# Performance work log

Measured on AMD Instinct MI355X. Metric: run time of the kernel, lower is better.

The kernel has to match this reference:

```python
import jax, jax.numpy as jnp
import numpy as np

N, E, F_IN, HID, K, CLS = 50000, 800000, 512, 128, 4, 40
EPS = 0.3


def setup_inputs() -> dict:
    key = jax.random.key(0)
    ks = jax.random.split(key, 6)
    x = jax.random.normal(ks[0], (N, F_IN), dtype=jnp.float32)
    edge_index = jax.random.randint(ks[1], (2, E), 0, N, dtype=jnp.int32)
    # xavier_normal with gain=1.414 ~ gain*sqrt(2/(fan_in+fan_out))
    t1_w = jax.random.normal(ks[2], (HID, F_IN), jnp.float32) * (1.414 * np.sqrt(2.0 / (F_IN + HID)))
    t1_b = jnp.zeros((HID,), jnp.float32)
    gate_w = jax.random.normal(ks[3], (K, 2 * HID), jnp.float32) * (1.414 * np.sqrt(2.0 / (2 * HID + 1)))
    gate_b = jnp.zeros((K,), jnp.float32)
    t2_w = jax.random.normal(ks[4], (CLS, HID), jnp.float32) * (1.414 * np.sqrt(2.0 / (HID + CLS)))
    t2_b = jnp.zeros((CLS,), jnp.float32)
    return dict(x=x, edge_index=edge_index, t1_w=t1_w, t1_b=t1_b,
                gate_w=gate_w, gate_b=gate_b, t2_w=t2_w, t2_b=t2_b)


def _fa_layer(h, row, col, nd, gw, gb):
    # gate(cat[h_row, h_col]) as two matvecs (equivalent to concat + Linear)
    d = h.shape[1]
    g = jnp.tanh(h[row] @ gw[:d] + h[col] @ gw[d:] + gb)   # [E]
    norm = g * nd[row] * nd[col]                           # [E]
    msg = norm[:, None] * h[row]                           # x_j = h[source], [E, HID]
    # aggregate (add) into target nodes
    return jax.ops.segment_sum(msg, col, num_segments=h.shape[0])


def reference(x, edge_index, t1_w, t1_b, gate_w, gate_b, t2_w, t2_b):
    row, col = edge_index[0], edge_index[1]
    deg = jax.ops.segment_sum(jnp.ones((E,), x.dtype), row, num_segments=N)
    nd = jnp.clip(deg, 1.0, None) ** -0.5                  # degree^{-1/2}, clamped at 1
    h = jax.nn.relu(x @ t1_w.T + t1_b)                     # [N, HID]
    raw = h
    for k in range(K):
        h = EPS * raw + _fa_layer(h, row, col, nd, gate_w[k], gate_b[k])
    return jax.nn.log_softmax(h @ t2_w.T + t2_b, axis=1)   # [N, CLS]
```

## Files before the change

kernel.cpp:

```cpp
#include <hip/hip_runtime.h>
#include <math.h>

#define N_NODES 50000
#define N_EDGES 800000
#define F_IN    512
#define HID     128
#define K_LAYERS 4
#define N_CLS   40
#define EPS_C   0.3f
#define CAP     64

#define GB_BLOCKS 391
#define PB_BLOCKS 3125

typedef __bf16 bf16x8 __attribute__((ext_vector_type(8)));
typedef float  f32x4  __attribute__((ext_vector_type(4)));
typedef float  f32x2  __attribute__((ext_vector_type(2)));

__device__ inline unsigned short bfb(float f) {
    __bf16 b = (__bf16)f;
    return __builtin_bit_cast(unsigned short, b);
}
__device__ inline unsigned pack2(float a, float b) {
    return (unsigned)bfb(a) | ((unsigned)bfb(b) << 16);
}
__device__ inline float lo2(unsigned v) { return __builtin_bit_cast(float, v << 16); }
__device__ inline float hi2(unsigned v) { return __builtin_bit_cast(float, v & 0xffff0000u); }
__device__ inline bf16x8 ld_frag(const unsigned short* p) {
    uint4 q = *(const uint4*)p;
    return __builtin_bit_cast(bf16x8, q);
}
__device__ inline void acc_fp8(float g, uint2 v, float* acc) {
    f32x2 p0 = __builtin_amdgcn_cvt_pk_f32_fp8((int)v.x, false);
    f32x2 p1 = __builtin_amdgcn_cvt_pk_f32_fp8((int)v.x, true);
    f32x2 p2 = __builtin_amdgcn_cvt_pk_f32_fp8((int)v.y, false);
    f32x2 p3 = __builtin_amdgcn_cvt_pk_f32_fp8((int)v.y, true);
    acc[0] = fmaf(g, p0[0], acc[0]); acc[1] = fmaf(g, p0[1], acc[1]);
    acc[2] = fmaf(g, p1[0], acc[2]); acc[3] = fmaf(g, p1[1], acc[3]);
    acc[4] = fmaf(g, p2[0], acc[4]); acc[5] = fmaf(g, p2[1], acc[5]);
    acc[6] = fmaf(g, p3[0], acc[6]); acc[7] = fmaf(g, p3[1], acc[7]);
}

#define GS 72
__global__ __launch_bounds__(256) void k_gemm_prep(const float* __restrict__ x,
                                                   const float* __restrict__ w,
                                                   const float* __restrict__ bias,
                                                   unsigned* __restrict__ h0b,
                                                   unsigned short* __restrict__ h08,
                                                   const int* __restrict__ row,
                                                   const int* __restrict__ col,
                                                   int* __restrict__ deg,
                                                   int* __restrict__ cur,
                                                   int* __restrict__ bucket) {
    if (blockIdx.x >= GB_BLOCKS) {
        int e = (blockIdx.x - GB_BLOCKS) * 256 + threadIdx.x;
        if (e < N_EDGES) {
            int r = row[e], c = col[e];
            atomicAdd(&deg[r], 1);
            int p = atomicAdd(&cur[c], 1);
            if (p < CAP) bucket[((size_t)c << 6) + p] = r;
        }
        return;
    }

    __shared__ __attribute__((aligned(16))) unsigned short As[128 * GS];
    __shared__ __attribute__((aligned(16))) unsigned short Bs[128 * GS];
    const int t    = threadIdx.x;
    const int lane = t & 63;
    const int wv   = t >> 6;
    const int wrow = wv >> 1;
    const int wcol = wv & 1;
    const int nb0  = blockIdx.x * 128;
    const int m16  = lane & 15;
    const int quad = lane >> 4;

    f32x4 acc[4][4];
#pragma unroll
    for (int mi = 0; mi < 4; mi++)
#pragma unroll
        for (int ni = 0; ni < 4; ni++) acc[mi][ni] = (f32x4){0.f, 0.f, 0.f, 0.f};

    for (int k0 = 0; k0 < F_IN; k0 += 64) {
        __syncthreads();
        {
            int r  = t & 127;
            int kh = (t >> 7) * 32;
            int n  = nb0 + r;
            unsigned short* pl = &As[r * GS + kh];
            if (n < N_NODES) {
                const float* px = &x[(size_t)n * F_IN + k0 + kh];
#pragma unroll
                for (int q = 0; q < 4; q++) {
                    float4 f0 = *(const float4*)(px + q * 8);
                    float4 f1 = *(const float4*)(px + q * 8 + 4);
                    *(ushort4*)(pl + q * 8)     = make_ushort4(bfb(f0.x), bfb(f0.y), bfb(f0.z), bfb(f0.w));
                    *(ushort4*)(pl + q * 8 + 4) = make_ushort4(bfb(f1.x), bfb(f1.y), bfb(f1.z), bfb(f1.w));
                }
            } else {
#pragma unroll
                for (int q = 0; q < 8; q++) *(ushort4*)(pl + q * 4) = make_ushort4(0, 0, 0, 0);
            }
        }
        {
            int j  = t & 127;
            int kh = (t >> 7) * 32;
            const float* pw = &w[(size_t)j * F_IN + k0 + kh];
            unsigned short* pl = &Bs[j * GS + kh];
#pragma unroll
            for (int q = 0; q < 4; q++) {
                float4 f0 = *(const float4*)(pw + q * 8);
                float4 f1 = *(const float4*)(pw + q * 8 + 4);
                *(ushort4*)(pl + q * 8)     = make_ushort4(bfb(f0.x), bfb(f0.y), bfb(f0.z), bfb(f0.w));
                *(ushort4*)(pl + q * 8 + 4) = make_ushort4(bfb(f1.x), bfb(f1.y), bfb(f1.z), bfb(f1.w));
            }
        }
        __syncthreads();
#pragma unroll
        for (int kk = 0; kk < 64; kk += 32) {
            bf16x8 af[4], bfr[4];
#pragma unroll
            for (int mi = 0; mi < 4; mi++)
                af[mi] = ld_frag(&As[(wrow * 64 + mi * 16 + m16) * GS + kk + quad * 8]);
#pragma unroll
            for (int ni = 0; ni < 4; ni++)
                bfr[ni] = ld_frag(&Bs[(wcol * 64 + ni * 16 + m16) * GS + kk + quad * 8]);
#pragma unroll
            for (int mi = 0; mi < 4; mi++)
#pragma unroll
                for (int ni = 0; ni < 4; ni++)
                    acc[mi][ni] = __builtin_amdgcn_mfma_f32_16x16x32_bf16(af[mi], bfr[ni], acc[mi][ni], 0, 0, 0);
        }
    }
    float bj[4];
#pragma unroll
    for (int ni = 0; ni < 4; ni++) bj[ni] = bias[wcol * 64 + ni * 16 + m16];
    unsigned short* h0u = (unsigned short*)h0b;
    unsigned char*  h8u = (unsigned char*)h08;
#pragma unroll
    for (int mi = 0; mi < 4; mi++)
#pragma unroll
        for (int reg = 0; reg < 4; reg++) {
            int n = nb0 + wrow * 64 + mi * 16 + quad * 4 + reg;
            if (n < N_NODES) {
#pragma unroll
                for (int ni = 0; ni < 4; ni++) {
                    float v = fmaxf(acc[mi][ni][reg] + bj[ni], 0.f);
                    int f = wcol * 64 + ni * 16 + m16;
                    h0u[(size_t)n * HID + f] = bfb(v);
                    int pk = __builtin_amdgcn_cvt_pk_fp8_f32(v, v, 0, false);
                    h8u[(size_t)n * HID + f] = (unsigned char)(pk & 0xff);
                }
            }
        }
}

__global__ __launch_bounds__(256) void k_gate0(const unsigned* __restrict__ h0b,
                                               const int* __restrict__ deg,
                                               const float* __restrict__ gw,
                                               float2* __restrict__ pn0,
                                               float* __restrict__ bn0) {
    const int node = blockIdx.x * 4 + (threadIdx.x >> 6);
    const int lane = threadIdx.x & 63;
    if (node >= N_NODES) return;
    unsigned v = h0b[((size_t)node << 6) + lane];
    float hx = lo2(v), hy = hi2(v);
    float pa = hx * gw[2 * lane]       + hy * gw[2 * lane + 1];
    float pb = hx * gw[128 + 2 * lane] + hy * gw[129 + 2 * lane];
#pragma unroll
    for (int d = 32; d > 0; d >>= 1) {
        pa += __shfl_xor(pa, d);
        pb += __shfl_xor(pb, d);
    }
    if (lane == 0) {
        float dv = fmaxf((float)deg[node], 1.0f);
        pn0[node] = make_float2(pa, 1.0f / sqrtf(dv));
        bn0[node] = pb;
    }
}

#define ISSUE_GRP(BASE, A, B, C, D)                                  \
    {                                                                \
        int ea = __shfl(idx, (BASE) + esub);                         \
        int eb = __shfl(idx, (BASE) + esub + 4);                     \
        int ec = __shfl(idx, (BASE) + esub + 8);                     \
        int ed = __shfl(idx, (BASE) + esub + 12);                    \
        A = h8v[(size_t)ea * 16 + fg];                               \
        B = h8v[(size_t)eb * 16 + fg];                               \
        C = h8v[(size_t)ec * 16 + fg];                               \
        D = h8v[(size_t)ed * 16 + fg];                               \
    }

__global__ __launch_bounds__(256) void k_agg7(const unsigned short* __restrict__ h8,
                                              const unsigned* __restrict__ h0b,
                                              const float2* __restrict__ pn,
                                              const float* __restrict__ bn,
                                              const int* __restrict__ bucket,
                                              const int* __restrict__ cur,
                                              const float* __restrict__ gb_all, int k,
                                              unsigned short* __restrict__ out8,
                                              unsigned* __restrict__ out16,
                                              const float* __restrict__ gwn,
                                              float2* __restrict__ pnn,
                                              float* __restrict__ bnn) {
    const int node = blockIdx.x * 4 + (threadIdx.x >> 6);
    const int lane = threadIdx.x & 63;
    if (node >= N_NODES) return;
    const int esub = lane >> 4;
    const int fg   = lane & 15;

    const int    cntr = cur[node];
    int          idx  = bucket[((size_t)node << 6) + lane];
    const float2 pno  = pn[node];
    const float  bwr  = bn[node];
    uint4 h0v = ((const uint4*)h0b)[(size_t)node * 16 + fg];

    const int   cnt = min(cntr, CAP);
    if (lane >= cnt) idx = 0;
    const float ndc = pno.y;
    const float bw  = bwr + gb_all[k];

    const uint2* h8v = (const uint2*)h8;
    uint2 v0 = make_uint2(0, 0), v1 = v0, v2 = v0, v3 = v0;
    uint2 w0 = v0, w1 = v0, w2 = v0, w3 = v0;
    if (cnt > 0)  ISSUE_GRP(0,  v0, v1, v2, v3);
    if (cnt > 16) ISSUE_GRP(16, w0, w1, w2, w3);

    float g = 0.f;
    if (lane < cnt) {
        float2 pr = pn[idx];
        float tt = pr.x + bw;
        float ex = __expf(tt + tt);
        g = (1.f - 2.f / (ex + 1.f)) * pr.y * ndc;
    }

    float acc[8];
#pragma unroll
    for (int j = 0; j < 8; j++) acc[j] = 0.f;

    for (int base = 0; base < cnt; base += 16) {
        float g0 = __shfl(g, base + esub);
        float g1 = __shfl(g, base + esub + 4);
        float g2 = __shfl(g, base + esub + 8);
        float g3 = __shfl(g, base + esub + 12);
        uint2 c0 = v0, c1 = v1, c2 = v2, c3 = v3;
        v0 = w0; v1 = w1; v2 = w2; v3 = w3;
        if (base + 32 < cnt) ISSUE_GRP(base + 32, w0, w1, w2, w3);
        acc_fp8(g0, c0, acc);
        acc_fp8(g1, c1, acc);
        acc_fp8(g2, c2, acc);
        acc_fp8(g3, c3, acc);
    }

#pragma unroll
    for (int j = 0; j < 8; j++) {
        acc[j] += __shfl_xor(acc[j], 16);
        acc[j] += __shfl_xor(acc[j], 32);
    }

    float of[8];
    of[0] = fmaf(EPS_C, lo2(h0v.x), acc[0]); of[1] = fmaf(EPS_C, hi2(h0v.x), acc[1]);
    of[2] = fmaf(EPS_C, lo2(h0v.y), acc[2]); of[3] = fmaf(EPS_C, hi2(h0v.y), acc[3]);
    of[4] = fmaf(EPS_C, lo2(h0v.z), acc[4]); of[5] = fmaf(EPS_C, hi2(h0v.z), acc[5]);
    of[6] = fmaf(EPS_C, lo2(h0v.w), acc[6]); of[7] = fmaf(EPS_C, hi2(h0v.w), acc[7]);
    if (esub == 0) {
        if (gwn) {
            int p0 = __builtin_amdgcn_cvt_pk_fp8_f32(of[0], of[1], 0, false);
            p0     = __builtin_amdgcn_cvt_pk_fp8_f32(of[2], of[3], p0, true);
            int p1 = __builtin_amdgcn_cvt_pk_fp8_f32(of[4], of[5], 0, false);
            p1     = __builtin_amdgcn_cvt_pk_fp8_f32(of[6], of[7], p1, true);
            ((uint2*)out8)[(size_t)node * 16 + fg] = make_uint2((unsigned)p0, (unsigned)p1);
        } else {
            uint4 ov;
            ov.x = pack2(of[0], of[1]); ov.y = pack2(of[2], of[3]);
            ov.z = pack2(of[4], of[5]); ov.w = pack2(of[6], of[7]);
            ((uint4*)out16)[(size_t)node * 16 + fg] = ov;
        }
    }

    if (gwn) {
        const float4* gw4 = (const float4*)gwn;
        float4 wa0 = gw4[fg * 2], wa1 = gw4[fg * 2 + 1];
        float4 wb0 = gw4[32 + fg * 2], wb1 = gw4[32 + fg * 2 + 1];
        float pa = of[0] * wa0.x + of[1] * wa0.y + of[2] * wa0.z + of[3] * wa0.w
                 + of[4] * wa1.x + of[5] * wa1.y + of[6] * wa1.z + of[7] * wa1.w;
        float pb = of[0] * wb0.x + of[1] * wb0.y + of[2] * wb0.z + of[3] * wb0.w
                 + of[4] * wb1.x + of[5] * wb1.y + of[6] * wb1.z + of[7] * wb1.w;
#pragma unroll
        for (int d = 1; d <= 8; d <<= 1) {
            pa += __shfl_xor(pa, d);
            pb += __shfl_xor(pb, d);
        }
        if (lane == 0) { pnn[node] = make_float2(pa, ndc); bnn[node] = pb; }
    }
}

#define OB_BLOCKS 3125
__global__ __launch_bounds__(256) void k_out(const unsigned* __restrict__ hb,
                                             const float* __restrict__ w2,
                                             const float* __restrict__ b2,
                                             float* __restrict__ out) {
    __shared__ float ws[N_CLS][HID + 1];
    __shared__ float hs[4][HID];
    __shared__ float bs[N_CLS];
    const int t = threadIdx.x;
    for (int i = t; i < N_CLS * HID; i += 256) {
        ws[i / HID][i % HID] = w2[i];
    }
    if (t < N_CLS) bs[t] = b2[t];
    __syncthreads();
    const int wv = t >> 6, lane = t & 63;
#pragma unroll
    for (int it = 0; it < 4; it++) {
        const int node = blockIdx.x * 16 + wv * 4 + it;
        unsigned v = hb[((size_t)node << 6) + lane];
        hs[wv][2 * lane]     = lo2(v);
        hs[wv][2 * lane + 1] = hi2(v);
        float z = -INFINITY;
        if (lane < N_CLS) {
            float s = bs[lane];
#pragma unroll 8
            for (int kk = 0; kk < HID; kk++) s = fmaf(hs[wv][kk], ws[lane][kk], s);
            z = s;
        }
        float mx = z;
#pragma unroll
        for (int d = 32; d > 0; d >>= 1) mx = fmaxf(mx, __shfl_xor(mx, d));
        float ex = (z == -INFINITY) ? 0.f : expf(z - mx);
        float sum = ex;
#pragma unroll
        for (int d = 32; d > 0; d >>= 1) sum += __shfl_xor(sum, d);
        if (lane < N_CLS)
            out[(size_t)node * N_CLS + lane] = z - mx - logf(sum);
    }
}

extern "C" void kernel_launch(void* const* d_in, const int* in_sizes, int n_in,
                              void* d_out, int out_size, void* d_ws, size_t ws_size,
                              hipStream_t stream) {
    const float* x   = (const float*)d_in[0];
    const int*   ei  = (const int*)d_in[1];
    const float* t1w = (const float*)d_in[2];
    const float* t1b = (const float*)d_in[3];
    const float* gw  = (const float*)d_in[4];
    const float* gb  = (const float*)d_in[5];
    const float* t2w = (const float*)d_in[6];
    const float* t2b = (const float*)d_in[7];
    float* out = (float*)d_out;

    const int* row = ei;
    const int* col = ei + N_EDGES;

    char* p = (char*)d_ws;
    auto alloc = [&](size_t bytes) -> char* {
        char* q = p;
        p += (bytes + 255) & ~(size_t)255;
        return q;
    };
    unsigned*       h0b  = (unsigned*)alloc(sizeof(unsigned) * (size_t)N_NODES * 64);
    unsigned*       hF   = (unsigned*)alloc(sizeof(unsigned) * (size_t)N_NODES * 64);
    unsigned short* h08  = (unsigned short*)alloc(sizeof(unsigned short) * (size_t)N_NODES * 64);
    unsigned short* hA8  = (unsigned short*)alloc(sizeof(unsigned short) * (size_t)N_NODES * 64);
    unsigned short* hB8  = (unsigned short*)alloc(sizeof(unsigned short) * (size_t)N_NODES * 64);
    float2*         pn0  = (float2*)alloc(sizeof(float2) * N_NODES);
    float2*         pn1  = (float2*)alloc(sizeof(float2) * N_NODES);
    float*          bn0  = (float*)alloc(sizeof(float) * N_NODES);
    float*          bn1  = (float*)alloc(sizeof(float) * N_NODES);
    int*            degi = (int*)alloc(sizeof(int) * N_NODES);
    int*            cur  = (int*)alloc(sizeof(int) * N_NODES);
    int*            bucket = (int*)alloc(sizeof(int) * (size_t)N_NODES * CAP);

    hipMemsetAsync(degi, 0, sizeof(int) * N_NODES, stream);
    hipMemsetAsync(cur,  0, sizeof(int) * N_NODES, stream);

    const int wb = (N_NODES + 3) / 4;

    k_gemm_prep<<<GB_BLOCKS + PB_BLOCKS, 256, 0, stream>>>(x, t1w, t1b, h0b, h08,
                                                           row, col, degi, cur, bucket);
    k_gate0<<<wb, 256, 0, stream>>>(h0b, degi, gw, pn0, bn0);

    const unsigned short* hc8 = h08;
    unsigned short* ring8[2] = {hA8, hB8};
    const float2* pc = pn0;  float2* pnx = pn1;
    const float*  bc = bn0;  float*  bnx = bn1;
    for (int k = 0; k < K_LAYERS; k++) {
        const float* gwn = (k + 1 < K_LAYERS) ? (gw + (size_t)(k + 1) * 2 * HID) : nullptr;
        unsigned short* hn8 = ring8[k & 1];
        k_agg7<<<wb, 256, 0, stream>>>(hc8, h0b, pc, bc, bucket, cur, gb, k,
                                       hn8, hF, gwn, pnx, bnx);
        hc8 = hn8;
        const float2* tp = pc; pc = pnx; pnx = (float2*)tp;
        const float*  tb = bc; bc = bnx; bnx = (float*)tb;
    }

    k_out<<<OB_BLOCKS, 256, 0, stream>>>(hF, t2w, t2b, out);
}
```

Before: 400.8 us.

## Split edge prep into own kernel and fuse layer-0 gate projection into GEMM epilogue

Moves edge degree/bucket construction out of the GEMM kernel into a separate kernel that handles two edges per thread. Shrinks the GEMM tile from 128 to 64 rows, doubling the number of blocks. Computes the layer-0 gate dot products in the GEMM epilogue with shuffles and shared-memory atomics, which removes the separate k_gate0 launch and its re-read of h0. The cost is that prep and GEMM now run one after the other instead of overlapping inside one launch, and the smaller tile reloads the weight tile more often.

```diff
diff --git a/kernel.cpp b/kernel.cpp
--- a/kernel.cpp
+++ b/kernel.cpp
@@ -10,8 +10,8 @@
 #define EPS_C   0.3f
 #define CAP     64
 
-#define GB_BLOCKS 391
-#define PB_BLOCKS 3125
+#define GB_BLOCKS 782
+#define PB_BLOCKS 1563
 
 typedef __bf16 bf16x8 __attribute__((ext_vector_type(8)));
 typedef float  f32x4  __attribute__((ext_vector_type(4)));
@@ -41,56 +41,65 @@
     acc[6] = fmaf(g, p3[0], acc[6]); acc[7] = fmaf(g, p3[1], acc[7]);
 }
 
+__global__ __launch_bounds__(256) void k_prep(const int* __restrict__ row,
+                                              const int* __restrict__ col,
+                                              int* __restrict__ deg,
+                                              int* __restrict__ cur,
+                                              int* __restrict__ bucket) {
+    int e0 = (blockIdx.x * 256 + threadIdx.x) * 2;
+    if (e0 >= N_EDGES) return;
+    int2 r2 = *(const int2*)&row[e0];
+    int2 c2 = *(const int2*)&col[e0];
+    atomicAdd(&deg[r2.x], 1);
+    atomicAdd(&deg[r2.y], 1);
+    int p0 = atomicAdd(&cur[c2.x], 1);
+    int p1 = atomicAdd(&cur[c2.y], 1);
+    if (p0 < CAP) bucket[((size_t)c2.x << 6) + p0] = r2.x;
+    if (p1 < CAP) bucket[((size_t)c2.y << 6) + p1] = r2.y;
+}
+
 #define GS 72
-__global__ __launch_bounds__(256) void k_gemm_prep(const float* __restrict__ x,
-                                                   const float* __restrict__ w,
-                                                   const float* __restrict__ bias,
-                                                   unsigned* __restrict__ h0b,
-                                                   unsigned short* __restrict__ h08,
-                                                   const int* __restrict__ row,
-                                                   const int* __restrict__ col,
-                                                   int* __restrict__ deg,
-                                                   int* __restrict__ cur,
-                                                   int* __restrict__ bucket) {
-    if (blockIdx.x >= GB_BLOCKS) {
-        int e = (blockIdx.x - GB_BLOCKS) * 256 + threadIdx.x;
-        if (e < N_EDGES) {
-            int r = row[e], c = col[e];
-            atomicAdd(&deg[r], 1);
-            int p = atomicAdd(&cur[c], 1);
-            if (p < CAP) bucket[((size_t)c << 6) + p] = r;
-        }
-        return;
-    }
-
-    __shared__ __attribute__((aligned(16))) unsigned short As[128 * GS];
+__global__ __launch_bounds__(256) void k_gemm(const float* __restrict__ x,
+                                              const float* __restrict__ w,
+                                              const float* __restrict__ bias,
+                                              const float* __restrict__ gw,
+                                              const int* __restrict__ deg,
+                                              unsigned* __restrict__ h0b,
+                                              unsigned short* __restrict__ h08,
+                                              float2* __restrict__ pn0,
+                                              float* __restrict__ bn0) {
+    __shared__ __attribute__((aligned(16))) unsigned short As[64 * GS];
     __shared__ __attribute__((aligned(16))) unsigned short Bs[128 * GS];
+    __shared__ float redA[64];
+    __shared__ float redB[64];
     const int t    = threadIdx.x;
     const int lane = t & 63;
     const int wv   = t >> 6;
     const int wrow = wv >> 1;
     const int wcol = wv & 1;
-    const int nb0  = blockIdx.x * 128;
+    const int nb0  = blockIdx.x * 64;
     const int m16  = lane & 15;
     const int quad = lane >> 4;
 
-    f32x4 acc[4][4];
-#pragma unroll
-    for (int mi = 0; mi < 4; mi++)
+    if (t < 64) { redA[t] = 0.f; redB[t] = 0.f; }
+
+    f32x4 acc[2][4];
+#pragma unroll
+    for (int mi = 0; mi < 2; mi++)
 #pragma unroll
         for (int ni = 0; ni < 4; ni++) acc[mi][ni] = (f32x4){0.f, 0.f, 0.f, 0.f};
 
     for (int k0 = 0; k0 < F_IN; k0 += 64) {
         __syncthreads();
         {
-            int r  = t & 127;
-            int kh = (t >> 7) * 32;
+            int r  = t & 63;
+            int kh = (t >> 6) * 16;
             int n  = nb0 + r;
             unsigned short* pl = &As[r * GS + kh];
             if (n < N_NODES) {
                 const float* px = &x[(size_t)n * F_IN + k0 + kh];
 #pragma unroll
-                for (int q = 0; q < 4; q++) {
+                for (int q = 0; q < 2; q++) {
                     float4 f0 = *(const float4*)(px + q * 8);
                     float4 f1 = *(const float4*)(px + q * 8 + 4);
                     *(ushort4*)(pl + q * 8)     = make_ushort4(bfb(f0.x), bfb(f0.y), bfb(f0.z), bfb(f0.w));
@@ -98,7 +107,7 @@
                 }
             } else {
 #pragma unroll
-                for (int q = 0; q < 8; q++) *(ushort4*)(pl + q * 4) = make_ushort4(0, 0, 0, 0);
+                for (int q = 0; q < 4; q++) *(ushort4*)(pl + q * 4) = make_ushort4(0, 0, 0, 0);
             }
         }
         {
@@ -117,30 +126,37 @@
         __syncthreads();
 #pragma unroll
         for (int kk = 0; kk < 64; kk += 32) {
-            bf16x8 af[4], bfr[4];
-#pragma unroll
-            for (int mi = 0; mi < 4; mi++)
-                af[mi] = ld_frag(&As[(wrow * 64 + mi * 16 + m16) * GS + kk + quad * 8]);
+            bf16x8 af[2], bfr[4];
+#pragma unroll
+            for (int mi = 0; mi < 2; mi++)
+                af[mi] = ld_frag(&As[(wrow * 32 + mi * 16 + m16) * GS + kk + quad * 8]);
 #pragma unroll
             for (int ni = 0; ni < 4; ni++)
                 bfr[ni] = ld_frag(&Bs[(wcol * 64 + ni * 16 + m16) * GS + kk + quad * 8]);
 #pragma unroll
-            for (int mi = 0; mi < 4; mi++)
+            for (int mi = 0; mi < 2; mi++)
 #pragma unroll
                 for (int ni = 0; ni < 4; ni++)
                     acc[mi][ni] = __builtin_amdgcn_mfma_f32_16x16x32_bf16(af[mi], bfr[ni], acc[mi][ni], 0, 0, 0);
         }
     }
-    float bj[4];
-#pragma unroll
-    for (int ni = 0; ni < 4; ni++) bj[ni] = bias[wcol * 64 + ni * 16 + m16];
+    float bj[4], ga[4], gb2[4];
+#pragma unroll
+    for (int ni = 0; ni < 4; ni++) {
+        int f = wcol * 64 + ni * 16 + m16;
+        bj[ni]  = bias[f];
+        ga[ni]  = gw[f];
+        gb2[ni] = gw[128 + f];
+    }
     unsigned short* h0u = (unsigned short*)h0b;
     unsigned char*  h8u = (unsigned char*)h08;
 #pragma unroll
-    for (int mi = 0; mi < 4; mi++)
+    for (int mi = 0; mi < 2; mi++)
 #pragma unroll
         for (int reg = 0; reg < 4; reg++) {
-            int n = nb0 + wrow * 64 + mi * 16 + quad * 4 + reg;
+            int loc = wrow * 32 + mi * 16 + quad * 4 + reg;
+            int n   = nb0 + loc;
+            float pa = 0.f, pb = 0.f;
             if (n < N_NODES) {
 #pragma unroll
                 for (int ni = 0; ni < 4; ni++) {
@@ -149,32 +165,28 @@
                     h0u[(size_t)n * HID + f] = bfb(v);
                     int pk = __builtin_amdgcn_cvt_pk_fp8_f32(v, v, 0, false);
                     h8u[(size_t)n * HID + f] = (unsigned char)(pk & 0xff);
+                    pa = fmaf(v, ga[ni], pa);
+                    pb = fmaf(v, gb2[ni], pb);
                 }
             }
-        }
-}
-
-__global__ __launch_bounds__(256) void k_gate0(const unsigned* __restrict__ h0b,
-                                               const int* __restrict__ deg,
-                                               const float* __restrict__ gw,
-                                               float2* __restrict__ pn0,
-                                               float* __restrict__ bn0) {
-    const int node = blockIdx.x * 4 + (threadIdx.x >> 6);
-    const int lane = threadIdx.x & 63;
-    if (node >= N_NODES) return;
-    unsigned v = h0b[((size_t)node << 6) + lane];
-    float hx = lo2(v), hy = hi2(v);
-    float pa = hx * gw[2 * lane]       + hy * gw[2 * lane + 1];
-    float pb = hx * gw[128 + 2 * lane] + hy * gw[129 + 2 * lane];
-#pragma unroll
-    for (int d = 32; d > 0; d >>= 1) {
-        pa += __shfl_xor(pa, d);
-        pb += __shfl_xor(pb, d);
-    }
-    if (lane == 0) {
-        float dv = fmaxf((float)deg[node], 1.0f);
-        pn0[node] = make_float2(pa, 1.0f / sqrtf(dv));
-        bn0[node] = pb;
+#pragma unroll
+            for (int d = 1; d <= 8; d <<= 1) {
+                pa += __shfl_xor(pa, d);
+                pb += __shfl_xor(pb, d);
+            }
+            if (m16 == 0) {
+                atomicAdd(&redA[loc], pa);
+                atomicAdd(&redB[loc], pb);
+            }
+        }
+    __syncthreads();
+    if (t < 64) {
+        int n = nb0 + t;
+        if (n < N_NODES) {
+            float dv = fmaxf((float)deg[n], 1.0f);
+            pn0[n] = make_float2(redA[t], 1.0f / sqrtf(dv));
+            bn0[n] = redB[t];
+        }
     }
 }
 
@@ -374,9 +386,8 @@
 
     const int wb = (N_NODES + 3) / 4;
 
-    k_gemm_prep<<<GB_BLOCKS + PB_BLOCKS, 256, 0, stream>>>(x, t1w, t1b, h0b, h08,
-                                                           row, col, degi, cur, bucket);
-    k_gate0<<<wb, 256, 0, stream>>>(h0b, degi, gw, pn0, bn0);
+    k_prep<<<PB_BLOCKS, 256, 0, stream>>>(row, col, degi, cur, bucket);
+    k_gemm<<<GB_BLOCKS, 256, 0, stream>>>(x, t1w, t1b, gw, degi, h0b, h08, pn0, bn0);
 
     const unsigned short* hc8 = h08;
     unsigned short* ring8[2] = {hA8, hB8};
```

Result: slower. 462.5 us (+15.4%).

## Fuse propagation layers and output head into one cooperative persistent kernel

Applied to the files above, without the earlier changes.

Replaces the four per-layer aggregation launches plus the output kernel with a single cooperative persistent kernel that uses grid-wide syncs between layers, prefetches the next node's metadata, and fuses the final linear+log_softmax into the last layer. The GEMM now writes fp32 and a separate kernel converts to bf16/fp8 and computes the first gate projections. This aims to remove launch gaps and the hF round trip, at the cost of grid.sync overhead, a reduced grid size, and an extra fp32 write and read of h0.

```diff
diff --git a/kernel.cpp b/kernel.cpp
--- a/kernel.cpp
+++ b/kernel.cpp
@@ -1,5 +1,8 @@
 #include <hip/hip_runtime.h>
+#include <hip/hip_cooperative_groups.h>
 #include <math.h>
+
+namespace cg = cooperative_groups;
 
 #define N_NODES 50000
 #define N_EDGES 800000
@@ -45,8 +48,7 @@
 __global__ __launch_bounds__(256) void k_gemm_prep(const float* __restrict__ x,
                                                    const float* __restrict__ w,
                                                    const float* __restrict__ bias,
-                                                   unsigned* __restrict__ h0b,
-                                                   unsigned short* __restrict__ h08,
+                                                   float* __restrict__ h0,
                                                    const int* __restrict__ row,
                                                    const int* __restrict__ col,
                                                    int* __restrict__ deg,
@@ -134,8 +136,6 @@
     float bj[4];
 #pragma unroll
     for (int ni = 0; ni < 4; ni++) bj[ni] = bias[wcol * 64 + ni * 16 + m16];
-    unsigned short* h0u = (unsigned short*)h0b;
-    unsigned char*  h8u = (unsigned char*)h08;
 #pragma unroll
     for (int mi = 0; mi < 4; mi++)
 #pragma unroll
@@ -143,29 +143,29 @@
             int n = nb0 + wrow * 64 + mi * 16 + quad * 4 + reg;
             if (n < N_NODES) {
 #pragma unroll
-                for (int ni = 0; ni < 4; ni++) {
-                    float v = fmaxf(acc[mi][ni][reg] + bj[ni], 0.f);
-                    int f = wcol * 64 + ni * 16 + m16;
-                    h0u[(size_t)n * HID + f] = bfb(v);
-                    int pk = __builtin_amdgcn_cvt_pk_fp8_f32(v, v, 0, false);
-                    h8u[(size_t)n * HID + f] = (unsigned char)(pk & 0xff);
-                }
-            }
-        }
-}
-
-__global__ __launch_bounds__(256) void k_gate0(const unsigned* __restrict__ h0b,
-                                               const int* __restrict__ deg,
-                                               const float* __restrict__ gw,
-                                               float2* __restrict__ pn0,
-                                               float* __restrict__ bn0) {
+                for (int ni = 0; ni < 4; ni++)
+                    h0[(size_t)n * HID + wcol * 64 + ni * 16 + m16] =
+                        fmaxf(acc[mi][ni][reg] + bj[ni], 0.f);
+            }
+        }
+}
+
+__global__ __launch_bounds__(256) void k_h2b_ab(const float* __restrict__ raw,
+                                                const int* __restrict__ deg,
+                                                const float* __restrict__ gw,
+                                                unsigned* __restrict__ h0b,
+                                                unsigned short* __restrict__ h08,
+                                                float2* __restrict__ pn0,
+                                                float* __restrict__ bn0) {
     const int node = blockIdx.x * 4 + (threadIdx.x >> 6);
     const int lane = threadIdx.x & 63;
     if (node >= N_NODES) return;
-    unsigned v = h0b[((size_t)node << 6) + lane];
-    float hx = lo2(v), hy = hi2(v);
-    float pa = hx * gw[2 * lane]       + hy * gw[2 * lane + 1];
-    float pb = hx * gw[128 + 2 * lane] + hy * gw[129 + 2 * lane];
+    float2 hv = ((const float2*)raw)[((size_t)node << 6) + lane];
+    h0b[((size_t)node << 6) + lane] = pack2(hv.x, hv.y);
+    int f8 = __builtin_amdgcn_cvt_pk_fp8_f32(hv.x, hv.y, 0, false);
+    h08[((size_t)node << 6) + lane] = (unsigned short)(f8 & 0xffff);
+    float pa = hv.x * gw[2 * lane]       + hv.y * gw[2 * lane + 1];
+    float pb = hv.x * gw[128 + 2 * lane] + hv.y * gw[129 + 2 * lane];
 #pragma unroll
     for (int d = 32; d > 0; d >>= 1) {
         pa += __shfl_xor(pa, d);
@@ -180,15 +180,186 @@
 
 #define ISSUE_GRP(BASE, A, B, C, D)                                  \
     {                                                                \
-        int ea = __shfl(idx, (BASE) + esub);                         \
-        int eb = __shfl(idx, (BASE) + esub + 4);                     \
-        int ec = __shfl(idx, (BASE) + esub + 8);                     \
-        int ed = __shfl(idx, (BASE) + esub + 12);                    \
+        int ea = __shfl(id, (BASE) + esub);                          \
+        int eb = __shfl(id, (BASE) + esub + 4);                      \
+        int ec = __shfl(id, (BASE) + esub + 8);                      \
+        int ed = __shfl(id, (BASE) + esub + 12);                     \
         A = h8v[(size_t)ea * 16 + fg];                               \
         B = h8v[(size_t)eb * 16 + fg];                               \
         C = h8v[(size_t)ec * 16 + fg];                               \
         D = h8v[(size_t)ed * 16 + fg];                               \
     }
+
+__global__ __launch_bounds__(256, 4) void k_net(
+        const unsigned short* __restrict__ h08,
+        unsigned short* __restrict__ hA8,
+        unsigned short* __restrict__ hB8,
+        const unsigned* __restrict__ h0b,
+        float2* __restrict__ pn0, float2* __restrict__ pn1,
+        float* __restrict__ bn0, float* __restrict__ bn1,
+        const int* __restrict__ bucket,
+        const int* __restrict__ cur,
+        const float* __restrict__ gw,
+        const float* __restrict__ gb,
+        const float* __restrict__ w2,
+        const float* __restrict__ b2,
+        float* __restrict__ out) {
+    cg::grid_group grid = cg::this_grid();
+    __shared__ float ws[N_CLS][HID + 1];
+    __shared__ float bs[N_CLS];
+    __shared__ float hs[4][HID];
+    const int t = threadIdx.x;
+    for (int i = t; i < N_CLS * HID; i += 256) ws[i >> 7][i & 127] = w2[i];
+    if (t < N_CLS) bs[t] = b2[t];
+
+    const int wv   = t >> 6;
+    const int lane = t & 63;
+    const int esub = lane >> 4;
+    const int fg   = lane & 15;
+    const int npb  = (N_NODES + gridDim.x - 1) / gridDim.x;
+    const int nb0  = blockIdx.x * npb;
+    const int nbE  = min(nb0 + npb, N_NODES);
+
+    for (int k = 0; k < K_LAYERS; k++) {
+        const unsigned short* src8 = (k == 0) ? h08 : ((k == 2) ? hB8 : hA8);
+        unsigned short*       dst8 = (k == 1) ? hB8 : hA8;
+        const float2* pc  = (k & 1) ? pn1 : pn0;
+        float2*       pnx = (k & 1) ? pn0 : pn1;
+        const float*  bc  = (k & 1) ? bn1 : bn0;
+        float*        bnx = (k & 1) ? bn0 : bn1;
+        const float   gbk = gb[k];
+        const float*  gwn = (k < 3) ? (gw + (size_t)(k + 1) * 2 * HID) : nullptr;
+        const uint2*  h8v = (const uint2*)src8;
+
+        int node = nb0 + wv;
+        int cntr = 0, idx = 0;
+        float2 pno = make_float2(0.f, 0.f);
+        float  bwr = 0.f;
+        uint4  h0v = make_uint4(0, 0, 0, 0);
+        if (node < nbE) {
+            cntr = cur[node];
+            idx  = bucket[((size_t)node << 6) + lane];
+            pno  = pc[node];
+            bwr  = bc[node];
+            h0v  = ((const uint4*)h0b)[(size_t)node * 16 + fg];
+        }
+
+        while (node < nbE) {
+            const int nnode = node + 4;
+            int cntrN = 0, idxN = 0;
+            float2 pnoN = make_float2(0.f, 0.f);
+            float  bwrN = 0.f;
+            uint4  h0vN = make_uint4(0, 0, 0, 0);
+            if (nnode < nbE) {
+                cntrN = cur[nnode];
+                idxN  = bucket[((size_t)nnode << 6) + lane];
+                pnoN  = pc[nnode];
+                bwrN  = bc[nnode];
+                h0vN  = ((const uint4*)h0b)[(size_t)nnode * 16 + fg];
+            }
+
+            const int   cnt = min(cntr, CAP);
+            int         id  = (lane < cnt) ? idx : 0;
+            const float ndc = pno.y;
+            const float bw  = bwr + gbk;
+
+            uint2 v0 = make_uint2(0, 0), v1 = v0, v2 = v0, v3 = v0;
+            uint2 u0 = v0, u1 = v0, u2 = v0, u3 = v0;
+            if (cnt > 0)  ISSUE_GRP(0,  v0, v1, v2, v3);
+            if (cnt > 16) ISSUE_GRP(16, u0, u1, u2, u3);
+
+            float g = 0.f;
+            if (lane < cnt) {
+                float2 pr = pc[id];
+                float tt = pr.x + bw;
+                float ex = __expf(tt + tt);
+                g = (1.f - 2.f / (ex + 1.f)) * pr.y * ndc;
+            }
+
+            float acc[8];
+#pragma unroll
+            for (int j = 0; j < 8; j++) acc[j] = 0.f;
+
+            for (int base = 0; base < cnt; base += 16) {
+                float g0 = __shfl(g, base + esub);
+                float g1 = __shfl(g, base + esub + 4);
+                float g2 = __shfl(g, base + esub + 8);
+                float g3 = __shfl(g, base + esub + 12);
+                uint2 c0 = v0, c1 = v1, c2 = v2, c3 = v3;
+                v0 = u0; v1 = u1; v2 = u2; v3 = u3;
+                if (base + 32 < cnt) ISSUE_GRP(base + 32, u0, u1, u2, u3);
+                acc_fp8(g0, c0, acc);
+                acc_fp8(g1, c1, acc);
+                acc_fp8(g2, c2, acc);
+                acc_fp8(g3, c3, acc);
+            }
+
+#pragma unroll
+            for (int j = 0; j < 8; j++) {
+                acc[j] += __shfl_xor(acc[j], 16);
+                acc[j] += __shfl_xor(acc[j], 32);
+            }
+
+            float of[8];
+            of[0] = fmaf(EPS_C, lo2(h0v.x), acc[0]); of[1] = fmaf(EPS_C, hi2(h0v.x), acc[1]);
+            of[2] = fmaf(EPS_C, lo2(h0v.y), acc[2]); of[3] = fmaf(EPS_C, hi2(h0v.y), acc[3]);
+            of[4] = fmaf(EPS_C, lo2(h0v.z), acc[4]); of[5] = fmaf(EPS_C, hi2(h0v.z), acc[5]);
+            of[6] = fmaf(EPS_C, lo2(h0v.w), acc[6]); of[7] = fmaf(EPS_C, hi2(h0v.w), acc[7]);
+
+            if (gwn) {
+                if (esub == 0) {
+                    int p0 = __builtin_amdgcn_cvt_pk_fp8_f32(of[0], of[1], 0, false);
+                    p0     = __builtin_amdgcn_cvt_pk_fp8_f32(of[2], of[3], p0, true);
+                    int p1 = __builtin_amdgcn_cvt_pk_fp8_f32(of[4], of[5], 0, false);
+                    p1     = __builtin_amdgcn_cvt_pk_fp8_f32(of[6], of[7], p1, true);
+                    ((uint2*)dst8)[(size_t)node * 16 + fg] = make_uint2((unsigned)p0, (unsigned)p1);
+                }
+                const float4* gw4 = (const float4*)gwn;
+                float4 wa0 = gw4[fg * 2], wa1 = gw4[fg * 2 + 1];
+                float4 wb0 = gw4[32 + fg * 2], wb1 = gw4[32 + fg * 2 + 1];
+                float pa = of[0] * wa0.x + of[1] * wa0.y + of[2] * wa0.z + of[3] * wa0.w
+                         + of[4] * wa1.x + of[5] * wa1.y + of[6] * wa1.z + of[7] * wa1.w;
+                float pb = of[0] * wb0.x + of[1] * wb0.y + of[2] * wb0.z + of[3] * wb0.w
+                         + of[4] * wb1.x + of[5] * wb1.y + of[6] * wb1.z + of[7] * wb1.w;
+#pragma unroll
+                for (int d = 1; d <= 8; d <<= 1) {
+                    pa += __shfl_xor(pa, d);
+                    pb += __shfl_xor(pb, d);
+                }
+                if (lane == 0) { pnx[node] = make_float2(pa, ndc); bnx[node] = pb; }
+            } else {
+                if (esub == 0) {
+#pragma unroll
+                    for (int j = 0; j < 8; j++) hs[wv][fg * 8 + j] = of[j];
+                }
+                float z = -INFINITY;
+                if (lane < N_CLS) {
+                    float s = bs[lane];
+#pragma unroll 8
+                    for (int kk = 0; kk < HID; kk++) s = fmaf(hs[wv][kk], ws[lane][kk], s);
+                    z = s;
+                }
+                float mx = z;
+#pragma unroll
+                for (int d = 32; d > 0; d >>= 1) mx = fmaxf(mx, __shfl_xor(mx, d));
+                float ex2 = (z == -INFINITY) ? 0.f : expf(z - mx);
+                float sum = ex2;
+#pragma unroll
+                for (int d = 32; d > 0; d >>= 1) sum += __shfl_xor(sum, d);
+                if (lane < N_CLS)
+                    out[(size_t)node * N_CLS + lane] = z - mx - logf(sum);
+            }
+
+            node = nnode;
+            cntr = cntrN; idx = idxN; pno = pnoN; bwr = bwrN; h0v = h0vN;
+        }
+
+        if (k < K_LAYERS - 1) {
+            __threadfence();
+            grid.sync();
+        }
+    }
+}
 
 __global__ __launch_bounds__(256) void k_agg7(const unsigned short* __restrict__ h8,
                                               const unsigned* __restrict__ h0b,
@@ -215,19 +386,19 @@
     uint4 h0v = ((const uint4*)h0b)[(size_t)node * 16 + fg];
 
     const int   cnt = min(cntr, CAP);
-    if (lane >= cnt) idx = 0;
+    int         id  = (lane < cnt) ? idx : 0;
     const float ndc = pno.y;
     const float bw  = bwr + gb_all[k];
 
     const uint2* h8v = (const uint2*)h8;
     uint2 v0 = make_uint2(0, 0), v1 = v0, v2 = v0, v3 = v0;
-    uint2 w0 = v0, w1 = v0, w2 = v0, w3 = v0;
+    uint2 u0 = v0, u1 = v0, u2 = v0, u3 = v0;
     if (cnt > 0)  ISSUE_GRP(0,  v0, v1, v2, v3);
-    if (cnt > 16) ISSUE_GRP(16, w0, w1, w2, w3);
+    if (cnt > 16) ISSUE_GRP(16, u0, u1, u2, u3);
 
     float g = 0.f;
     if (lane < cnt) {
-        float2 pr = pn[idx];
+        float2 pr = pn[id];
         float tt = pr.x + bw;
         float ex = __expf(tt + tt);
         g = (1.f - 2.f / (ex + 1.f)) * pr.y * ndc;
@@ -243,8 +414,8 @@
         float g2 = __shfl(g, base + esub + 8);
         float g3 = __shfl(g, base + esub + 12);
         uint2 c0 = v0, c1 = v1, c2 = v2, c3 = v3;
-        v0 = w0; v1 = w1; v2 = w2; v3 = w3;
-        if (base + 32 < cnt) ISSUE_GRP(base + 32, w0, w1, w2, w3);
+        v0 = u0; v1 = u1; v2 = u2; v3 = u3;
+        if (base + 32 < cnt) ISSUE_GRP(base + 32, u0, u1, u2, u3);
         acc_fp8(g0, c0, acc);
         acc_fp8(g1, c1, acc);
         acc_fp8(g2, c2, acc);
@@ -294,7 +465,6 @@
     }
 }
 
-#define OB_BLOCKS 3125
 __global__ __launch_bounds__(256) void k_out(const unsigned* __restrict__ hb,
                                              const float* __restrict__ w2,
                                              const float* __restrict__ b2,
@@ -307,31 +477,30 @@
         ws[i / HID][i % HID] = w2[i];
     }
     if (t < N_CLS) bs[t] = b2[t];
-    __syncthreads();
-    const int wv = t >> 6, lane = t & 63;
-#pragma unroll
-    for (int it = 0; it < 4; it++) {
-        const int node = blockIdx.x * 16 + wv * 4 + it;
+    int wv = t >> 6, lane = t & 63;
+    int node = blockIdx.x * 4 + wv;
+    if (node < N_NODES) {
         unsigned v = hb[((size_t)node << 6) + lane];
         hs[wv][2 * lane]     = lo2(v);
         hs[wv][2 * lane + 1] = hi2(v);
-        float z = -INFINITY;
-        if (lane < N_CLS) {
-            float s = bs[lane];
+    }
+    __syncthreads();
+    float z = -INFINITY;
+    if (node < N_NODES && lane < N_CLS) {
+        float s = bs[lane];
 #pragma unroll 8
-            for (int kk = 0; kk < HID; kk++) s = fmaf(hs[wv][kk], ws[lane][kk], s);
-            z = s;
-        }
-        float mx = z;
-#pragma unroll
-        for (int d = 32; d > 0; d >>= 1) mx = fmaxf(mx, __shfl_xor(mx, d));
-        float ex = (z == -INFINITY) ? 0.f : expf(z - mx);
-        float sum = ex;
-#pragma unroll
-        for (int d = 32; d > 0; d >>= 1) sum += __shfl_xor(sum, d);
-        if (lane < N_CLS)
-            out[(size_t)node * N_CLS + lane] = z - mx - logf(sum);
-    }
+        for (int kk = 0; kk < HID; kk++) s = fmaf(hs[wv][kk], ws[lane][kk], s);
+        z = s;
+    }
+    float mx = z;
+#pragma unroll
+    for (int d = 32; d > 0; d >>= 1) mx = fmaxf(mx, __shfl_xor(mx, d));
+    float ex = (z == -INFINITY) ? 0.f : expf(z - mx);
+    float sum = ex;
+#pragma unroll
+    for (int d = 32; d > 0; d >>= 1) sum += __shfl_xor(sum, d);
+    if (node < N_NODES && lane < N_CLS)
+        out[(size_t)node * N_CLS + lane] = z - mx - logf(sum);
 }
 
 extern "C" void kernel_launch(void* const* d_in, const int* in_sizes, int n_in,
@@ -356,6 +525,7 @@
         p += (bytes + 255) & ~(size_t)255;
         return q;
     };
+    float*          raw  = (float*)alloc(sizeof(float) * (size_t)N_NODES * HID);
     unsigned*       h0b  = (unsigned*)alloc(sizeof(unsigned) * (size_t)N_NODES * 64);
     unsigned*       hF   = (unsigned*)alloc(sizeof(unsigned) * (size_t)N_NODES * 64);
     unsigned short* h08  = (unsigned short*)alloc(sizeof(unsigned short) * (size_t)N_NODES * 64);
@@ -374,23 +544,44 @@
 
     const int wb = (N_NODES + 3) / 4;
 
-    k_gemm_prep<<<GB_BLOCKS + PB_BLOCKS, 256, 0, stream>>>(x, t1w, t1b, h0b, h08,
+    k_gemm_prep<<<GB_BLOCKS + PB_BLOCKS, 256, 0, stream>>>(x, t1w, t1b, raw,
                                                            row, col, degi, cur, bucket);
-    k_gate0<<<wb, 256, 0, stream>>>(h0b, degi, gw, pn0, bn0);
-
-    const unsigned short* hc8 = h08;
-    unsigned short* ring8[2] = {hA8, hB8};
-    const float2* pc = pn0;  float2* pnx = pn1;
-    const float*  bc = bn0;  float*  bnx = bn1;
-    for (int k = 0; k < K_LAYERS; k++) {
-        const float* gwn = (k + 1 < K_LAYERS) ? (gw + (size_t)(k + 1) * 2 * HID) : nullptr;
-        unsigned short* hn8 = ring8[k & 1];
-        k_agg7<<<wb, 256, 0, stream>>>(hc8, h0b, pc, bc, bucket, cur, gb, k,
-                                       hn8, hF, gwn, pnx, bnx);
-        hc8 = hn8;
-        const float2* tp = pc; pc = pnx; pnx = (float2*)tp;
-        const float*  tb = bc; bc = bnx; bnx = (float*)tb;
-    }
-
-    k_out<<<OB_BLOCKS, 256, 0, stream>>>(hF, t2w, t2b, out);
-}
+    k_h2b_ab<<<wb, 256, 0, stream>>>(raw, degi, gw, h0b, h08, pn0, bn0);
+
+    static int coop_blocks = -2;
+    if (coop_blocks == -2) {
+        int occ = 0;
+        hipError_t oe = hipOccupancyMaxActiveBlocksPerMultiprocessor(
+            &occ, (const void*)k_net, 256, 0);
+        coop_blocks = (oe == hipSuccess && occ > 0) ? (occ * 256) : 0;
+        if (coop_blocks > 2048) coop_blocks = 2048;
+    }
+
+    hipError_t ce = hipErrorUnknown;
+    if (coop_blocks > 0) {
+        void* args[] = {(void*)&h08, (void*)&hA8, (void*)&hB8, (void*)&h0b,
+                        (void*)&pn0, (void*)&pn1, (void*)&bn0, (void*)&bn1,
+                        (void*)&bucket, (void*)&cur, (void*)&gw, (void*)&gb,
+                        (void*)&t2w, (void*)&t2b, (void*)&out};
+        ce = hipLaunchCooperativeKernel((const void*)k_net, dim3(coop_blocks),
+                                        dim3(256), args, 0, stream);
+        if (ce != hipSuccess) coop_blocks = 0;
+    }
+
+    if (ce != hipSuccess) {
+        const unsigned short* hc8 = h08;
+        unsigned short* ring8[2] = {hA8, hB8};
+        const float2* pc = pn0;  float2* pnx = pn1;
+        const float*  bc = bn0;  float*  bnx = bn1;
+        for (int k = 0; k < K_LAYERS; k++) {
+            const float* gwn = (k + 1 < K_LAYERS) ? (gw + (size_t)(k + 1) * 2 * HID) : nullptr;
+            unsigned short* hn8 = ring8[k & 1];
+            k_agg7<<<wb, 256, 0, stream>>>(hc8, h0b, pc, bc, bucket, cur, gb, k,
+                                           hn8, hF, gwn, pnx, bnx);
+            hc8 = hn8;
+            const float2* tp = pc; pc = pnx; pnx = (float2*)tp;
+            const float*  tb = bc; bc = bnx; bnx = (float*)tb;
+        }
+        k_out<<<wb, 256, 0, stream>>>(hF, t2w, t2b, out);
+    }
+}
```

Result: slower. 835.3 us (+108.4%).

## Issue all neighbor gathers up front and move bf16/fp8 conversion out of GEMM

Applied to the files above, without the earlier changes.

The aggregation kernel now issues all four 16-edge gather groups (up to the 64-edge cap) before any accumulation. This replaces the two-deep rolling prefetch loop and gives more memory-level parallelism per wave, at the cost of extra registers. The GEMM epilogue now writes fp32 into a new raw buffer instead of scattered 2-byte and 1-byte stores. A renamed gate-prep kernel then converts raw to bf16 and fp8 with coalesced stores while computing the gate projections. This adds an extra fp32 write and read of the hidden matrix.

```diff
diff --git a/kernel.cpp b/kernel.cpp
--- a/kernel.cpp
+++ b/kernel.cpp
@@ -45,8 +45,7 @@
 __global__ __launch_bounds__(256) void k_gemm_prep(const float* __restrict__ x,
                                                    const float* __restrict__ w,
                                                    const float* __restrict__ bias,
-                                                   unsigned* __restrict__ h0b,
-                                                   unsigned short* __restrict__ h08,
+                                                   float* __restrict__ h0,
                                                    const int* __restrict__ row,
                                                    const int* __restrict__ col,
                                                    int* __restrict__ deg,
@@ -134,8 +133,6 @@
     float bj[4];
 #pragma unroll
     for (int ni = 0; ni < 4; ni++) bj[ni] = bias[wcol * 64 + ni * 16 + m16];
-    unsigned short* h0u = (unsigned short*)h0b;
-    unsigned char*  h8u = (unsigned char*)h08;
 #pragma unroll
     for (int mi = 0; mi < 4; mi++)
 #pragma unroll
@@ -143,29 +140,29 @@
             int n = nb0 + wrow * 64 + mi * 16 + quad * 4 + reg;
             if (n < N_NODES) {
 #pragma unroll
-                for (int ni = 0; ni < 4; ni++) {
-                    float v = fmaxf(acc[mi][ni][reg] + bj[ni], 0.f);
-                    int f = wcol * 64 + ni * 16 + m16;
-                    h0u[(size_t)n * HID + f] = bfb(v);
-                    int pk = __builtin_amdgcn_cvt_pk_fp8_f32(v, v, 0, false);
-                    h8u[(size_t)n * HID + f] = (unsigned char)(pk & 0xff);
-                }
+                for (int ni = 0; ni < 4; ni++)
+                    h0[(size_t)n * HID + wcol * 64 + ni * 16 + m16] =
+                        fmaxf(acc[mi][ni][reg] + bj[ni], 0.f);
             }
         }
 }
 
-__global__ __launch_bounds__(256) void k_gate0(const unsigned* __restrict__ h0b,
-                                               const int* __restrict__ deg,
-                                               const float* __restrict__ gw,
-                                               float2* __restrict__ pn0,
-                                               float* __restrict__ bn0) {
+__global__ __launch_bounds__(256) void k_h2b_ab(const float* __restrict__ raw,
+                                                const int* __restrict__ deg,
+                                                const float* __restrict__ gw,
+                                                unsigned* __restrict__ h0b,
+                                                unsigned short* __restrict__ h08,
+                                                float2* __restrict__ pn0,
+                                                float* __restrict__ bn0) {
     const int node = blockIdx.x * 4 + (threadIdx.x >> 6);
     const int lane = threadIdx.x & 63;
     if (node >= N_NODES) return;
-    unsigned v = h0b[((size_t)node << 6) + lane];
-    float hx = lo2(v), hy = hi2(v);
-    float pa = hx * gw[2 * lane]       + hy * gw[2 * lane + 1];
-    float pb = hx * gw[128 + 2 * lane] + hy * gw[129 + 2 * lane];
+    float2 hv = ((const float2*)raw)[((size_t)node << 6) + lane];
+    h0b[((size_t)node << 6) + lane] = pack2(hv.x, hv.y);
+    int f8 = __builtin_amdgcn_cvt_pk_fp8_f32(hv.x, hv.y, 0, false);
+    h08[((size_t)node << 6) + lane] = (unsigned short)(f8 & 0xffff);
+    float pa = hv.x * gw[2 * lane]       + hv.y * gw[2 * lane + 1];
+    float pb = hv.x * gw[128 + 2 * lane] + hv.y * gw[129 + 2 * lane];
 #pragma unroll
     for (int d = 32; d > 0; d >>= 1) {
         pa += __shfl_xor(pa, d);
@@ -180,17 +177,29 @@
 
 #define ISSUE_GRP(BASE, A, B, C, D)                                  \
     {                                                                \
-        int ea = __shfl(idx, (BASE) + esub);                         \
-        int eb = __shfl(idx, (BASE) + esub + 4);                     \
-        int ec = __shfl(idx, (BASE) + esub + 8);                     \
-        int ed = __shfl(idx, (BASE) + esub + 12);                    \
+        int ea = __shfl(id, (BASE) + esub);                          \
+        int eb = __shfl(id, (BASE) + esub + 4);                      \
+        int ec = __shfl(id, (BASE) + esub + 8);                      \
+        int ed = __shfl(id, (BASE) + esub + 12);                     \
         A = h8v[(size_t)ea * 16 + fg];                               \
         B = h8v[(size_t)eb * 16 + fg];                               \
         C = h8v[(size_t)ec * 16 + fg];                               \
         D = h8v[(size_t)ed * 16 + fg];                               \
     }
 
-__global__ __launch_bounds__(256) void k_agg7(const unsigned short* __restrict__ h8,
+#define ACC_GRP(BASE, A, B, C, D)                                    \
+    {                                                                \
+        float g0 = __shfl(g, (BASE) + esub);                         \
+        float g1 = __shfl(g, (BASE) + esub + 4);                     \
+        float g2 = __shfl(g, (BASE) + esub + 8);                     \
+        float g3 = __shfl(g, (BASE) + esub + 12);                    \
+        acc_fp8(g0, A, acc);                                         \
+        acc_fp8(g1, B, acc);                                         \
+        acc_fp8(g2, C, acc);                                         \
+        acc_fp8(g3, D, acc);                                         \
+    }
+
+__global__ __launch_bounds__(256) void k_agg8(const unsigned short* __restrict__ h8,
                                               const unsigned* __restrict__ h0b,
                                               const float2* __restrict__ pn,
                                               const float* __restrict__ bn,
@@ -215,19 +224,23 @@
     uint4 h0v = ((const uint4*)h0b)[(size_t)node * 16 + fg];
 
     const int   cnt = min(cntr, CAP);
-    if (lane >= cnt) idx = 0;
+    int         id  = (lane < cnt) ? idx : 0;
     const float ndc = pno.y;
     const float bw  = bwr + gb_all[k];
 
     const uint2* h8v = (const uint2*)h8;
-    uint2 v0 = make_uint2(0, 0), v1 = v0, v2 = v0, v3 = v0;
-    uint2 w0 = v0, w1 = v0, w2 = v0, w3 = v0;
-    if (cnt > 0)  ISSUE_GRP(0,  v0, v1, v2, v3);
-    if (cnt > 16) ISSUE_GRP(16, w0, w1, w2, w3);
+    uint2 a0 = make_uint2(0, 0), a1 = a0, a2 = a0, a3 = a0;
+    uint2 b0 = a0, b1 = a0, b2 = a0, b3 = a0;
+    uint2 c0 = a0, c1 = a0, c2 = a0, c3 = a0;
+    uint2 d0 = a0, d1 = a0, d2 = a0, d3 = a0;
+    if (cnt > 0)  ISSUE_GRP(0,  a0, a1, a2, a3);
+    if (cnt > 16) ISSUE_GRP(16, b0, b1, b2, b3);
+    if (cnt > 32) ISSUE_GRP(32, c0, c1, c2, c3);
+    if (cnt > 48) ISSUE_GRP(48, d0, d1, d2, d3);
 
     float g = 0.f;
     if (lane < cnt) {
-        float2 pr = pn[idx];
+        float2 pr = pn[id];
         float tt = pr.x + bw;
         float ex = __expf(tt + tt);
         g = (1.f - 2.f / (ex + 1.f)) * pr.y * ndc;
@@ -237,19 +250,10 @@
 #pragma unroll
     for (int j = 0; j < 8; j++) acc[j] = 0.f;
 
-    for (int base = 0; base < cnt; base += 16) {
-        float g0 = __shfl(g, base + esub);
-        float g1 = __shfl(g, base + esub + 4);
-        float g2 = __shfl(g, base + esub + 8);
-        float g3 = __shfl(g, base + esub + 12);
-        uint2 c0 = v0, c1 = v1, c2 = v2, c3 = v3;
-        v0 = w0; v1 = w1; v2 = w2; v3 = w3;
-        if (base + 32 < cnt) ISSUE_GRP(base + 32, w0, w1, w2, w3);
-        acc_fp8(g0, c0, acc);
-        acc_fp8(g1, c1, acc);
-        acc_fp8(g2, c2, acc);
-        acc_fp8(g3, c3, acc);
-    }
+    if (cnt > 0)  ACC_GRP(0,  a0, a1, a2, a3);
+    if (cnt > 16) ACC_GRP(16, b0, b1, b2, b3);
+    if (cnt > 32) ACC_GRP(32, c0, c1, c2, c3);
+    if (cnt > 48) ACC_GRP(48, d0, d1, d2, d3);
 
 #pragma unroll
     for (int j = 0; j < 8; j++) {
@@ -356,6 +360,7 @@
         p += (bytes + 255) & ~(size_t)255;
         return q;
     };
+    float*          raw  = (float*)alloc(sizeof(float) * (size_t)N_NODES * HID);
     unsigned*       h0b  = (unsigned*)alloc(sizeof(unsigned) * (size_t)N_NODES * 64);
     unsigned*       hF   = (unsigned*)alloc(sizeof(unsigned) * (size_t)N_NODES * 64);
     unsigned short* h08  = (unsigned short*)alloc(sizeof(unsigned short) * (size_t)N_NODES * 64);
@@ -374,9 +379,9 @@
 
     const int wb = (N_NODES + 3) / 4;
 
-    k_gemm_prep<<<GB_BLOCKS + PB_BLOCKS, 256, 0, stream>>>(x, t1w, t1b, h0b, h08,
+    k_gemm_prep<<<GB_BLOCKS + PB_BLOCKS, 256, 0, stream>>>(x, t1w, t1b, raw,
                                                            row, col, degi, cur, bucket);
-    k_gate0<<<wb, 256, 0, stream>>>(h0b, degi, gw, pn0, bn0);
+    k_h2b_ab<<<wb, 256, 0, stream>>>(raw, degi, gw, h0b, h08, pn0, bn0);
 
     const unsigned short* hc8 = h08;
     unsigned short* ring8[2] = {hA8, hB8};
@@ -385,7 +390,7 @@
     for (int k = 0; k < K_LAYERS; k++) {
         const float* gwn = (k + 1 < K_LAYERS) ? (gw + (size_t)(k + 1) * 2 * HID) : nullptr;
         unsigned short* hn8 = ring8[k & 1];
-        k_agg7<<<wb, 256, 0, stream>>>(hc8, h0b, pc, bc, bucket, cur, gb, k,
+        k_agg8<<<wb, 256, 0, stream>>>(hc8, h0b, pc, bc, bucket, cur, gb, k,
                                        hn8, hF, gwn, pnx, bnx);
         hc8 = hn8;
         const float2* tp = pc; pc = pnx; pnx = (float2*)tp;
```

Result: no change. 393.7 us (-1.8%).
